# Performance work log

Measured on AMD Instinct MI355X. Metric: run time of the kernel, lower is better.

## Reference

```python
import jax, jax.numpy as jnp
import numpy as np

N_NODES = 50000
N_EDGES = 800000
EMB = 100
LAYERS = 3
EPS = 1e-12  # torch F.normalize default eps


def setup_inputs() -> dict:
    key = jax.random.key(0)
    k1, k2, k3, k4 = jax.random.split(key, 4)
    adj_row = jax.random.randint(k1, (N_EDGES,), 0, N_NODES, dtype=jnp.int32)
    adj_col = jax.random.randint(k2, (N_EDGES,), 0, N_NODES, dtype=jnp.int32)
    adj_val = jax.random.uniform(k3, (N_EDGES,), dtype=jnp.float32)
    embedding = jax.random.normal(k4, (N_NODES, EMB), dtype=jnp.float32)
    a = jnp.ones((LAYERS + 1, 1, 1), dtype=jnp.float32)  # init.ones_
    return {"adj_row": adj_row, "adj_col": adj_col, "adj_val": adj_val,
            "embedding": embedding, "a": a}


def reference(adj_row, adj_col, adj_val, embedding, a):
    def spmm(x):
        # sparse.mm(A, x): gather source rows, scale by edge value, scatter-add to dest rows
        return jax.ops.segment_sum(adj_val[:, None] * x[adj_col], adj_row,
                                   num_segments=N_NODES)

    outs = [embedding]
    x = embedding
    for _ in range(LAYERS):
        x = spmm(x)
        outs.append(x)
    final = jnp.stack(outs, axis=0)  # [L+1, N, d]
    # F.normalize(..., dim=-1, p=2): x / max(||x||_2, eps)
    norm = jnp.sqrt(jnp.sum(final * final, axis=-1, keepdims=True))
    final = final / jnp.maximum(norm, EPS)
    return jnp.sum(a * final, axis=0)  # [N, d]
```

## Files before the change

kernel.cpp:

```cpp
#include <hip/hip_runtime.h>
#include <hip/hip_bf16.h>

#define N_NODES 50000
#define N_EDGES 800000
#define EMB 100
#define HALF_EMB 50
#define NORM_EPS 1e-12f
#define BROWS 128
#define NB ((N_NODES + BROWS - 1) / BROWS)
#define CAP 4096
#define EPB 4096

#define CONV_BLOCKS ((N_NODES + 3) / 4)

__global__ void bucket_scatter(const int* __restrict__ adj_row,
                               const int* __restrict__ adj_col,
                               const float* __restrict__ adj_val,
                               int* __restrict__ bucket_cnt,
                               int2* __restrict__ slab) {
    __shared__ int hist[NB];
    __shared__ int cur[NB];
    const int t = threadIdx.x;
    const int base_e = blockIdx.x * EPB;
    for (int i = t; i < NB; i += 256) hist[i] = 0;
    __syncthreads();
    int rows[EPB / 256];
    #pragma unroll
    for (int j = 0; j < EPB / 256; ++j) {
        int e = base_e + j * 256 + t;
        int r = (e < N_EDGES) ? adj_row[e] : -1;
        rows[j] = r;
        if (r >= 0) atomicAdd(&hist[r >> 7], 1);
    }
    __syncthreads();
    for (int i = t; i < NB; i += 256) {
        int c = hist[i];
        cur[i] = (c > 0) ? atomicAdd(&bucket_cnt[i], c) : 0;
    }
    __syncthreads();
    #pragma unroll
    for (int j = 0; j < EPB / 256; ++j) {
        int e = base_e + j * 256 + t;
        int r = rows[j];
        if (r >= 0) {
            int b = r >> 7;
            int p = atomicAdd(&cur[b], 1);
            unsigned rc = ((unsigned)r << 16) | (unsigned)adj_col[e];
            slab[(size_t)b * CAP + p] = make_int2((int)rc, __float_as_int(adj_val[e]));
        }
    }
}

__global__ void csr_build_conv(const int* __restrict__ bucket_cnt,
                               const int2* __restrict__ slab,
                               unsigned* __restrict__ csr4,
                               int* __restrict__ row_ptr,
                               const float* __restrict__ emb,
                               float* __restrict__ norm0,
                               __hip_bfloat162* __restrict__ xb) {
    __shared__ int2 eds[CAP];
    __shared__ int hist[BROWS];
    __shared__ int incl[BROWS];
    __shared__ int red[256];
    const int t = threadIdx.x;
    if (blockIdx.x >= NB) {
        int wave = (blockIdx.x - NB) * 4 + (t >> 6);
        int lane = t & 63;
        if (wave >= N_NODES) return;
        float2 v = make_float2(0.0f, 0.0f);
        size_t idx = (size_t)wave * HALF_EMB + lane;
        if (lane < HALF_EMB) v = ((const float2*)emb)[idx];
        float s = v.x * v.x + v.y * v.y;
        #pragma unroll
        for (int off = 32; off > 0; off >>= 1) s += __shfl_xor(s, off);
        if (lane == 0) norm0[wave] = sqrtf(s);
        if (lane < HALF_EMB) {
            __hip_bfloat162 b;
            b.x = __float2bfloat16(v.x);
            b.y = __float2bfloat16(v.y);
            xb[idx] = b;
        }
        return;
    }
    const int b = blockIdx.x;
    int part = 0;
    for (int i = t; i < b; i += 256) part += bucket_cnt[i];
    red[t] = part;
    __syncthreads();
    #pragma unroll
    for (int off = 128; off > 0; off >>= 1) {
        if (t < off) red[t] += red[t + off];
        __syncthreads();
    }
    const int base = red[0];
    const int cnt = bucket_cnt[b];
    for (int i = t; i < cnt; i += 256) eds[i] = slab[(size_t)b * CAP + i];
    if (t < BROWS) hist[t] = 0;
    __syncthreads();
    for (int i = t; i < cnt; i += 256)
        atomicAdd(&hist[(int)(((unsigned)eds[i].x) >> 16) & (BROWS - 1)], 1);
    __syncthreads();
    int v = (t < BROWS) ? hist[t] : 0;
    if (t < BROWS) incl[t] = v;
    __syncthreads();
    #pragma unroll
    for (int off = 1; off < BROWS; off <<= 1) {
        int n = (t >= off && t < BROWS) ? incl[t - off] : 0;
        __syncthreads();
        if (t < BROWS) incl[t] += n;
        __syncthreads();
    }
    int ex = (t < BROWS) ? (incl[t] - v) : 0;
    __syncthreads();
    if (t < BROWS) hist[t] = ex;
    int gr = b * BROWS + t;
    if (t < BROWS && gr < N_NODES) row_ptr[gr] = base + ex;
    if (b == 0 && t == 0) row_ptr[N_NODES] = N_EDGES;
    __syncthreads();
    for (int i = t; i < cnt; i += 256) {
        int2 e = eds[i];
        int l = (int)(((unsigned)e.x) >> 16) & (BROWS - 1);
        int p = atomicAdd(&hist[l], 1);
        unsigned col = (unsigned)e.x & 0xFFFFu;
        __hip_bfloat16 hv = __float2bfloat16(__int_as_float(e.y));
        unsigned vb = (unsigned)*reinterpret_cast<unsigned short*>(&hv);
        csr4[base + p] = (col << 16) | vb;
    }
}

__global__ void spmm_fused(const int* __restrict__ row_ptr,
                           const unsigned* __restrict__ csr4,
                           const __hip_bfloat162* __restrict__ xb,
                           __hip_bfloat162* __restrict__ yb,
                           float* __restrict__ norm_out,
                           const float* __restrict__ a,
                           const __hip_bfloat162* __restrict__ ep0,
                           const __hip_bfloat162* __restrict__ ep1,
                           const float* __restrict__ norms,
                           float* __restrict__ out,
                           int final_layer) {
    int wave = blockIdx.x * (blockDim.x >> 6) + (threadIdx.x >> 6);
    int lane = threadIdx.x & 63;
    if (wave >= N_NODES) return;
    int start = row_ptr[wave];
    int end   = row_ptr[wave + 1];
    int deg   = end - start;
    unsigned myrec = (lane < deg) ? csr4[start + lane] : 0u;
    bool act = (lane < HALF_EMB);
    float ax = 0.0f, ay = 0.0f;
    int dn = (deg < 64) ? deg : 64;
    int d = 0;
    for (; d + 3 < dn; d += 4) {
        unsigned r0 = __shfl(myrec, d);
        unsigned r1 = __shfl(myrec, d + 1);
        unsigned r2 = __shfl(myrec, d + 2);
        unsigned r3 = __shfl(myrec, d + 3);
        if (act) {
            __hip_bfloat162 p0 = xb[(size_t)(r0 >> 16) * HALF_EMB + lane];
            __hip_bfloat162 p1 = xb[(size_t)(r1 >> 16) * HALF_EMB + lane];
            __hip_bfloat162 p2 = xb[(size_t)(r2 >> 16) * HALF_EMB + lane];
            __hip_bfloat162 p3 = xb[(size_t)(r3 >> 16) * HALF_EMB + lane];
            float v0 = __uint_as_float(r0 << 16);
            float v1 = __uint_as_float(r1 << 16);
            float v2 = __uint_as_float(r2 << 16);
            float v3 = __uint_as_float(r3 << 16);
            ax += v0 * __bfloat162float(p0.x); ay += v0 * __bfloat162float(p0.y);
            ax += v1 * __bfloat162float(p1.x); ay += v1 * __bfloat162float(p1.y);
            ax += v2 * __bfloat162float(p2.x); ay += v2 * __bfloat162float(p2.y);
            ax += v3 * __bfloat162float(p3.x); ay += v3 * __bfloat162float(p3.y);
        }
    }
    for (; d < dn; ++d) {
        unsigned r = __shfl(myrec, d);
        if (act) {
            __hip_bfloat162 p = xb[(size_t)(r >> 16) * HALF_EMB + lane];
            float v = __uint_as_float(r << 16);
            ax += v * __bfloat162float(p.x);
            ay += v * __bfloat162float(p.y);
        }
    }
    for (int e = start + 64; e < end; ++e) {
        unsigned r = csr4[e];
        if (act) {
            __hip_bfloat162 p = xb[(size_t)(r >> 16) * HALF_EMB + lane];
            float v = __uint_as_float(r << 16);
            ax += v * __bfloat162float(p.x);
            ay += v * __bfloat162float(p.y);
        }
    }
    float s = ax * ax + ay * ay;
    #pragma unroll
    for (int off = 32; off > 0; off >>= 1) s += __shfl_xor(s, off);
    if (!final_layer) {
        if (act) {
            size_t idx = (size_t)wave * HALF_EMB + lane;
            __hip_bfloat162 bb;
            bb.x = __float2bfloat16(ax);
            bb.y = __float2bfloat16(ay);
            yb[idx] = bb;
        }
        if (lane == 0) norm_out[wave] = sqrtf(s);
    } else {
        float s0 = a[0] / fmaxf(norms[wave], NORM_EPS);
        float s1 = a[1] / fmaxf(norms[N_NODES + wave], NORM_EPS);
        float s2 = a[2] / fmaxf(norms[2 * N_NODES + wave], NORM_EPS);
        float s3 = a[3] / fmaxf(sqrtf(s), NORM_EPS);
        if (act) {
            size_t idx = (size_t)wave * HALF_EMB + lane;
            __hip_bfloat162 e0 = ep0[idx];
            __hip_bfloat162 e1 = ep1[idx];
            __hip_bfloat162 e2 = xb[idx];
            float2 o;
            o.x = s0 * __bfloat162float(e0.x) + s1 * __bfloat162float(e1.x)
                + s2 * __bfloat162float(e2.x) + s3 * ax;
            o.y = s0 * __bfloat162float(e0.y) + s1 * __bfloat162float(e1.y)
                + s2 * __bfloat162float(e2.y) + s3 * ay;
            ((float2*)out)[idx] = o;
        }
    }
}

extern "C" void kernel_launch(void* const* d_in, const int* in_sizes, int n_in,
                              void* d_out, int out_size, void* d_ws, size_t ws_size,
                              hipStream_t stream) {
    const int*   adj_row   = (const int*)d_in[0];
    const int*   adj_col   = (const int*)d_in[1];
    const float* adj_val   = (const float*)d_in[2];
    const float* embedding = (const float*)d_in[3];
    const float* a         = (const float*)d_in[4];
    float* out = (float*)d_out;

    int2* slab     = (int2*)d_ws;
    unsigned* csr4 = (unsigned*)(slab + (size_t)NB * CAP);
    __hip_bfloat162* xbE = (__hip_bfloat162*)(csr4 + N_EDGES);
    __hip_bfloat162* xb1 = xbE + (size_t)N_NODES * HALF_EMB;
    float* norms = (float*)(xb1 + (size_t)N_NODES * HALF_EMB);
    int* row_ptr    = (int*)(norms + 3 * N_NODES);
    int* bucket_cnt = row_ptr + (N_NODES + 1);
    __hip_bfloat162* xb2 = (__hip_bfloat162*)slab;

    const int node_blocks = (N_NODES + 3) / 4;
    const int part_blocks = (N_EDGES + EPB - 1) / EPB;

    hipMemsetAsync(bucket_cnt, 0, sizeof(int) * NB, stream);
    bucket_scatter<<<part_blocks, 256, 0, stream>>>(adj_row, adj_col, adj_val,
                                                    bucket_cnt, slab);
    csr_build_conv<<<NB + CONV_BLOCKS, 256, 0, stream>>>(bucket_cnt, slab, csr4,
                                                         row_ptr, embedding,
                                                         norms, xbE);

    spmm_fused<<<node_blocks, 256, 0, stream>>>(row_ptr, csr4, xbE, xb1,
                                                norms + N_NODES, a,
                                                nullptr, nullptr, nullptr,
                                                nullptr, 0);
    spmm_fused<<<node_blocks, 256, 0, stream>>>(row_ptr, csr4, xb1, xb2,
                                                norms + 2 * N_NODES, a,
                                                nullptr, nullptr, nullptr,
                                                nullptr, 0);
    spmm_fused<<<node_blocks, 256, 0, stream>>>(row_ptr, csr4, xb2, nullptr,
                                                nullptr, a,
                                                xbE, xb1, norms,
                                                out, 1);
}
```

Baseline: 225.2 us.

## Split wave into two half-waves each gathering a different edge with 8-byte loads

Each 64-lane wave now works as two 32-lane halves. Each half handles alternate edges and loads 4 bf16 features (uint2) per lane, using 25 lanes instead of 50 active lanes with 4-byte loads. The partial sums are combined with a cross-half shuffle before the norm and the store. The aim is to raise lane utilisation and issue fewer, wider gather loads per edge, at the cost of an extra reduction and of odd-degree padding on the tail.

```diff
diff --git a/kernel.cpp b/kernel.cpp
--- a/kernel.cpp
+++ b/kernel.cpp
@@ -5,6 +5,7 @@
 #define N_EDGES 800000
 #define EMB 100
 #define HALF_EMB 50
+#define QEMB 25
 #define NORM_EPS 1e-12f
 #define BROWS 128
 #define NB ((N_NODES + BROWS - 1) / BROWS)
@@ -128,14 +129,23 @@
     }
 }
 
+__device__ inline float4 up4(uint2 u) {
+    float4 f;
+    f.x = __uint_as_float(u.x << 16);
+    f.y = __uint_as_float(u.x & 0xFFFF0000u);
+    f.z = __uint_as_float(u.y << 16);
+    f.w = __uint_as_float(u.y & 0xFFFF0000u);
+    return f;
+}
+
 __global__ void spmm_fused(const int* __restrict__ row_ptr,
                            const unsigned* __restrict__ csr4,
-                           const __hip_bfloat162* __restrict__ xb,
-                           __hip_bfloat162* __restrict__ yb,
+                           const uint2* __restrict__ xb,
+                           uint2* __restrict__ yb,
                            float* __restrict__ norm_out,
                            const float* __restrict__ a,
-                           const __hip_bfloat162* __restrict__ ep0,
-                           const __hip_bfloat162* __restrict__ ep1,
+                           const uint2* __restrict__ ep0,
+                           const uint2* __restrict__ ep1,
                            const float* __restrict__ norms,
                            float* __restrict__ out,
                            int final_layer) {
@@ -146,58 +156,70 @@
     int end   = row_ptr[wave + 1];
     int deg   = end - start;
     unsigned myrec = (lane < deg) ? csr4[start + lane] : 0u;
-    bool act = (lane < HALF_EMB);
-    float ax = 0.0f, ay = 0.0f;
-    int dn = (deg < 64) ? deg : 64;
+    int h = lane >> 5, c = lane & 31;
+    bool act = (c < QEMB);
+    float4 acc = make_float4(0.0f, 0.0f, 0.0f, 0.0f);
+    int dn  = (deg < 64) ? deg : 64;
+    int dn2 = (dn + 1) & ~1;
     int d = 0;
-    for (; d + 3 < dn; d += 4) {
-        unsigned r0 = __shfl(myrec, d);
-        unsigned r1 = __shfl(myrec, d + 1);
-        unsigned r2 = __shfl(myrec, d + 2);
-        unsigned r3 = __shfl(myrec, d + 3);
+    for (; d + 8 <= dn2; d += 8) {
+        unsigned ra = __shfl(myrec, d + h);
+        unsigned rb = __shfl(myrec, d + 2 + h);
+        unsigned rc = __shfl(myrec, d + 4 + h);
+        unsigned rd = __shfl(myrec, d + 6 + h);
         if (act) {
-            __hip_bfloat162 p0 = xb[(size_t)(r0 >> 16) * HALF_EMB + lane];
-            __hip_bfloat162 p1 = xb[(size_t)(r1 >> 16) * HALF_EMB + lane];
-            __hip_bfloat162 p2 = xb[(size_t)(r2 >> 16) * HALF_EMB + lane];
-            __hip_bfloat162 p3 = xb[(size_t)(r3 >> 16) * HALF_EMB + lane];
-            float v0 = __uint_as_float(r0 << 16);
-            float v1 = __uint_as_float(r1 << 16);
-            float v2 = __uint_as_float(r2 << 16);
-            float v3 = __uint_as_float(r3 << 16);
-            ax += v0 * __bfloat162float(p0.x); ay += v0 * __bfloat162float(p0.y);
-            ax += v1 * __bfloat162float(p1.x); ay += v1 * __bfloat162float(p1.y);
-            ax += v2 * __bfloat162float(p2.x); ay += v2 * __bfloat162float(p2.y);
-            ax += v3 * __bfloat162float(p3.x); ay += v3 * __bfloat162float(p3.y);
-        }
-    }
-    for (; d < dn; ++d) {
-        unsigned r = __shfl(myrec, d);
+            uint2 ua = xb[(size_t)(ra >> 16) * QEMB + c];
+            uint2 ub = xb[(size_t)(rb >> 16) * QEMB + c];
+            uint2 uc = xb[(size_t)(rc >> 16) * QEMB + c];
+            uint2 ud = xb[(size_t)(rd >> 16) * QEMB + c];
+            float va = __uint_as_float(ra << 16);
+            float vb = __uint_as_float(rb << 16);
+            float vc = __uint_as_float(rc << 16);
+            float vd = __uint_as_float(rd << 16);
+            float4 fa = up4(ua), fb = up4(ub), fc = up4(uc), fd = up4(ud);
+            acc.x += va * fa.x; acc.y += va * fa.y; acc.z += va * fa.z; acc.w += va * fa.w;
+            acc.x += vb * fb.x; acc.y += vb * fb.y; acc.z += vb * fb.z; acc.w += vb * fb.w;
+            acc.x += vc * fc.x; acc.y += vc * fc.y; acc.z += vc * fc.z; acc.w += vc * fc.w;
+            acc.x += vd * fd.x; acc.y += vd * fd.y; acc.z += vd * fd.z; acc.w += vd * fd.w;
+        }
+    }
+    for (; d < dn2; d += 2) {
+        unsigned r = __shfl(myrec, d + h);
         if (act) {
-            __hip_bfloat162 p = xb[(size_t)(r >> 16) * HALF_EMB + lane];
+            uint2 u = xb[(size_t)(r >> 16) * QEMB + c];
             float v = __uint_as_float(r << 16);
-            ax += v * __bfloat162float(p.x);
-            ay += v * __bfloat162float(p.y);
-        }
-    }
-    for (int e = start + 64; e < end; ++e) {
-        unsigned r = csr4[e];
+            float4 f = up4(u);
+            acc.x += v * f.x; acc.y += v * f.y; acc.z += v * f.z; acc.w += v * f.w;
+        }
+    }
+    for (int e = start + 64; e < end; e += 2) {
+        unsigned r = (e + h < end) ? csr4[e + h] : 0u;
         if (act) {
-            __hip_bfloat162 p = xb[(size_t)(r >> 16) * HALF_EMB + lane];
+            uint2 u = xb[(size_t)(r >> 16) * QEMB + c];
             float v = __uint_as_float(r << 16);
-            ax += v * __bfloat162float(p.x);
-            ay += v * __bfloat162float(p.y);
-        }
-    }
-    float s = ax * ax + ay * ay;
+            float4 f = up4(u);
+            acc.x += v * f.x; acc.y += v * f.y; acc.z += v * f.z; acc.w += v * f.w;
+        }
+    }
+    acc.x += __shfl_xor(acc.x, 32);
+    acc.y += __shfl_xor(acc.y, 32);
+    acc.z += __shfl_xor(acc.z, 32);
+    acc.w += __shfl_xor(acc.w, 32);
+    float s = 0.0f;
+    if (h == 0 && act)
+        s = acc.x * acc.x + acc.y * acc.y + acc.z * acc.z + acc.w * acc.w;
     #pragma unroll
     for (int off = 32; off > 0; off >>= 1) s += __shfl_xor(s, off);
     if (!final_layer) {
-        if (act) {
-            size_t idx = (size_t)wave * HALF_EMB + lane;
-            __hip_bfloat162 bb;
-            bb.x = __float2bfloat16(ax);
-            bb.y = __float2bfloat16(ay);
-            yb[idx] = bb;
+        if (h == 0 && act) {
+            __hip_bfloat16 b0 = __float2bfloat16(acc.x);
+            __hip_bfloat16 b1 = __float2bfloat16(acc.y);
+            __hip_bfloat16 b2 = __float2bfloat16(acc.z);
+            __hip_bfloat16 b3 = __float2bfloat16(acc.w);
+            uint2 o;
+            o.x = (unsigned)*(unsigned short*)&b0 | ((unsigned)*(unsigned short*)&b1 << 16);
+            o.y = (unsigned)*(unsigned short*)&b2 | ((unsigned)*(unsigned short*)&b3 << 16);
+            yb[(size_t)wave * QEMB + c] = o;
         }
         if (lane == 0) norm_out[wave] = sqrtf(s);
     } else {
@@ -205,17 +227,17 @@
         float s1 = a[1] / fmaxf(norms[N_NODES + wave], NORM_EPS);
         float s2 = a[2] / fmaxf(norms[2 * N_NODES + wave], NORM_EPS);
         float s3 = a[3] / fmaxf(sqrtf(s), NORM_EPS);
-        if (act) {
-            size_t idx = (size_t)wave * HALF_EMB + lane;
-            __hip_bfloat162 e0 = ep0[idx];
-            __hip_bfloat162 e1 = ep1[idx];
-            __hip_bfloat162 e2 = xb[idx];
-            float2 o;
-            o.x = s0 * __bfloat162float(e0.x) + s1 * __bfloat162float(e1.x)
-                + s2 * __bfloat162float(e2.x) + s3 * ax;
-            o.y = s0 * __bfloat162float(e0.y) + s1 * __bfloat162float(e1.y)
-                + s2 * __bfloat162float(e2.y) + s3 * ay;
-            ((float2*)out)[idx] = o;
+        if (h == 0 && act) {
+            size_t idx = (size_t)wave * QEMB + c;
+            float4 f0 = up4(ep0[idx]);
+            float4 f1 = up4(ep1[idx]);
+            float4 f2 = up4(xb[idx]);
+            float4 o;
+            o.x = s0 * f0.x + s1 * f1.x + s2 * f2.x + s3 * acc.x;
+            o.y = s0 * f0.y + s1 * f1.y + s2 * f2.y + s3 * acc.y;
+            o.z = s0 * f0.z + s1 * f1.z + s2 * f2.z + s3 * acc.z;
+            o.w = s0 * f0.w + s1 * f1.w + s2 * f2.w + s3 * acc.w;
+            ((float4*)out)[idx] = o;
         }
     }
 }
@@ -232,12 +254,12 @@
 
     int2* slab     = (int2*)d_ws;
     unsigned* csr4 = (unsigned*)(slab + (size_t)NB * CAP);
-    __hip_bfloat162* xbE = (__hip_bfloat162*)(csr4 + N_EDGES);
-    __hip_bfloat162* xb1 = xbE + (size_t)N_NODES * HALF_EMB;
-    float* norms = (float*)(xb1 + (size_t)N_NODES * HALF_EMB);
+    uint2* xbE = (uint2*)(csr4 + N_EDGES);
+    uint2* xb1 = xbE + (size_t)N_NODES * QEMB;
+    float* norms = (float*)(xb1 + (size_t)N_NODES * QEMB);
     int* row_ptr    = (int*)(norms + 3 * N_NODES);
     int* bucket_cnt = row_ptr + (N_NODES + 1);
-    __hip_bfloat162* xb2 = (__hip_bfloat162*)slab;
+    uint2* xb2 = (uint2*)slab;
 
     const int node_blocks = (N_NODES + 3) / 4;
     const int part_blocks = (N_EDGES + EPB - 1) / EPB;
@@ -247,18 +269,18 @@
                                                     bucket_cnt, slab);
     csr_build_conv<<<NB + CONV_BLOCKS, 256, 0, stream>>>(bucket_cnt, slab, csr4,
                                                          row_ptr, embedding,
-                                                         norms, xbE);
-
-    spmm_fused<<<node_blocks, 256, 0, stream>>>(row_ptr, csr4, xbE, xb1,
-                                                norms + N_NODES, a,
+                                                         norms, (__hip_bfloat162*)xbE);
+
+    spmm_fused<<<node_blocks, 256, 0, stream>>>(row_ptr, csr4, xbE,
+                                                xb1, norms + N_NODES, a,
                                                 nullptr, nullptr, nullptr,
                                                 nullptr, 0);
-    spmm_fused<<<node_blocks, 256, 0, stream>>>(row_ptr, csr4, xb1, xb2,
-                                                norms + 2 * N_NODES, a,
+    spmm_fused<<<node_blocks, 256, 0, stream>>>(row_ptr, csr4, xb1,
+                                                xb2, norms + 2 * N_NODES, a,
                                                 nullptr, nullptr, nullptr,
                                                 nullptr, 0);
-    spmm_fused<<<node_blocks, 256, 0, stream>>>(row_ptr, csr4, xb2, nullptr,
-                                                nullptr, a,
+    spmm_fused<<<node_blocks, 256, 0, stream>>>(row_ptr, csr4, xb2,
+                                                nullptr, nullptr, a,
                                                 xbE, xb1, norms,
                                                 out, 1);
 }
```

Measured after the change: 216.9 us. -3.7%, faster.
